# Kernel tuning notes

Hardware: AMD Instinct MI355X
Metric: run time of the kernel (lower is better)

## Reference

```python
import jax, jax.numpy as jnp
import numpy as np

T, B, H = 1024, 128, 256


def setup_inputs() -> dict:
    key = jax.random.key(0)
    k1, k2, k3, k4, k5 = jax.random.split(key, 5)
    ins = jax.random.normal(k1, (T, B, H), dtype=jnp.float32)
    resets = jax.random.randint(k2, (T, B), 0, 2).astype(jnp.bool_)
    # GRUCell params (flax layout): input dense (with bias) and recurrent dense
    # (bias only on the candidate 'hn' branch). Orthogonal-ish init approximated
    # by scaled normal for a pure-jnp reference.
    s = 1.0 / np.sqrt(H)
    Wi = jax.random.normal(k3, (H, 3 * H), dtype=jnp.float32) * s   # -> [ir|iz|in]
    Wh = jax.random.normal(k4, (H, 3 * H), dtype=jnp.float32) * s   # -> [hr|hz|hn]
    bi = jnp.zeros((3 * H,), dtype=jnp.float32)
    bhn = jnp.zeros((H,), dtype=jnp.float32)
    h0 = jnp.zeros((B, H), dtype=jnp.float32)  # initialize_carry -> zeros
    return {"ins": ins, "resets": resets, "h0": h0,
            "Wi": Wi, "Wh": Wh, "bi": bi, "bhn": bhn}


def reference(ins, resets, h0, Wi, Wh, bi, bhn):
    """ScannedRNN: GRU recurrence over time with per-step reset masking.

    ins: [T,B,H], resets: [T,B] bool, h0: [B,H]. Returns (final_carry, ys).
    """
    Hh = h0.shape[-1]

    def step(h, xt):
        x_t, r_t = xt                              # [B,H], [B]
        h = jnp.where(r_t[:, None], 0.0, h)        # reset carry to zeros
        gi = x_t @ Wi + bi                         # [B,3H]
        gh = h @ Wh                                # [B,3H]
        i_r, i_z, i_n = gi[:, :Hh], gi[:, Hh:2 * Hh], gi[:, 2 * Hh:]
        h_r, h_z, h_n = gh[:, :Hh], gh[:, Hh:2 * Hh], gh[:, 2 * Hh:]
        r = jax.nn.sigmoid(i_r + h_r)
        z = jax.nn.sigmoid(i_z + h_z)
        n = jnp.tanh(i_n + r * (h_n + bhn))
        h_new = (1.0 - z) * n + z * h
        return h_new, h_new                        # GRUCell returns (carry, y=carry)

    h_final, ys = jax.lax.scan(step, h0, (ins, resets))
    return h_final, ys
```

## Files before the change

### kernel.cpp

```cpp
#include <hip/hip_runtime.h>


typedef _Float16 half2_t __attribute__((ext_vector_type(2)));
typedef _Float16 half4_t __attribute__((ext_vector_type(4)));
typedef _Float16 half8_t __attribute__((ext_vector_type(8)));
typedef float f32x4 __attribute__((ext_vector_type(4)));

#define T_DIM 1024
#define B_DIM 128
#define H_DIM 256
#define N3 768
#define NSTREAM 4096
#define ROWS 16

__device__ __forceinline__ int perm_n(int cp) {
  int ublk = cp / 48;
  int rem = cp % 48;
  int g = rem >> 4;
  int u4 = rem & 15;
  return g * 256 + ublk * 16 + u4;
}


__global__ void prep_whb(const float* __restrict__ Wh, unsigned* __restrict__ WhB) {
  int i = blockIdx.x * 256 + threadIdx.x;
  int h = 2 * i;
  int idx = h & 7;
  int lane = (h >> 3) & 63;
  int ntk = h >> 9;
  int nt = ntk % 48;
  int kt = ntk / 48;
  int k = kt * 32 + ((lane >> 4) * 8) + idx;
  int n = perm_n(nt * 16 + (lane & 15));
  half2_t p;
  p.x = (_Float16)Wh[(size_t)k * N3 + n];
  p.y = (_Float16)Wh[(size_t)(k + 1) * N3 + n];
  WhB[i] = __builtin_bit_cast(unsigned, p);
}

__global__ void prep_witp(const float* __restrict__ Wi, _Float16* __restrict__ WiTp) {
  int i = blockIdx.x * 256 + threadIdx.x;
  int cp = i >> 8;
  int k = i & 255;
  WiTp[(size_t)cp * 256 + k] = (_Float16)Wi[(size_t)k * N3 + perm_n(cp)];
}

__global__ void prep_bip(const float* __restrict__ bi, float* __restrict__ bip) {
  int i = threadIdx.x;
  bip[i] = bi[perm_n(i)];
}

__global__ void init_h(const float* __restrict__ h0, float* __restrict__ h_state) {
  int i = blockIdx.x * 256 + threadIdx.x;
  h_state[i] = h0[i];
}

__global__ __launch_bounds__(256) void conv_a(
    const float* __restrict__ src, _Float16* __restrict__ dst, int n8) {
  int i = blockIdx.x * 256 + threadIdx.x;
  const int stride = gridDim.x * 256;
  for (; i < n8; i += stride) {
    float4 a = ((const float4*)src)[2 * i];
    float4 b = ((const float4*)src)[2 * i + 1];
    half8_t h;
    h[0] = (_Float16)a.x; h[1] = (_Float16)a.y;
    h[2] = (_Float16)a.z; h[3] = (_Float16)a.w;
    h[4] = (_Float16)b.x; h[5] = (_Float16)b.y;
    h[6] = (_Float16)b.z; h[7] = (_Float16)b.w;
    ((half8_t*)dst)[i] = h;
  }
}


__global__ void seg_transpose(const int* __restrict__ resets, int* __restrict__ resT) {
  int i = blockIdx.x * 256 + threadIdx.x;
  int b = i >> 10;
  int t = i & 1023;
  resT[i] = resets[(size_t)t * B_DIM + b];
}

__global__ __launch_bounds__(256) void seg_extract(
    const int* __restrict__ resT, int t0, int steps,
    unsigned* __restrict__ rowsegs, unsigned* __restrict__ rowcnt,
    unsigned* __restrict__ lhist) {
  const int b = blockIdx.x;
  const int tid = threadIdx.x;
  const int lane = tid & 63;
  const int w = tid >> 6;
  const int per = (steps + 255) >> 8;

  __shared__ unsigned short sstartL[1025];
  __shared__ unsigned lcur[1025];
  __shared__ unsigned wsum[4];

  for (int l = tid; l <= steps; l += 256) lcur[l] = 0;

  const int* rrow = resT + (size_t)b * T_DIM + t0;
  int myfirst = tid * per;
  unsigned cnt = 0;
  for (int i = 0; i < per; ++i) {
    int s = myfirst + i;
    if (s < steps && (s == 0 || rrow[s] != 0)) cnt++;
  }
  unsigned pre = cnt;
#pragma unroll
  for (int off = 1; off < 64; off <<= 1) {
    unsigned v = __shfl_up(pre, off);
    if (lane >= off) pre += v;
  }
  if (lane == 63) wsum[w] = pre;
  __syncthreads();
  unsigned wbase = 0, total = 0;
#pragma unroll
  for (int i = 0; i < 4; ++i) {
    if (i < w) wbase += wsum[i];
    total += wsum[i];
  }
  unsigned r = wbase + pre - cnt;
  for (int i = 0; i < per; ++i) {
    int s = myfirst + i;
    if (s < steps && (s == 0 || rrow[s] != 0)) sstartL[r++] = (unsigned short)s;
  }
  if (tid == 0) { sstartL[total] = (unsigned short)steps; rowcnt[b] = total; }
  __syncthreads();

  const unsigned carry0 = (rrow[0] == 0) ? 1u : 0u;
  for (unsigned rr = tid; rr < total; rr += 256) {
    int st = sstartL[rr];
    int len = (int)sstartL[rr + 1] - st;
    unsigned carry = (st == 0) ? carry0 : 0u;
    unsigned rk = atomicAdd(&lcur[len], 1u);
    rowsegs[(size_t)b * T_DIM + rr] =
        (unsigned)st | ((unsigned)len << 10) | (rk << 21) | (carry << 31);
  }
  __syncthreads();
  for (int l = tid; l <= steps; l += 256) lhist[(size_t)l * 128 + b] = lcur[l];
}

__global__ __launch_bounds__(1024) void seg_prefix2(
    const unsigned* __restrict__ lhist, unsigned* __restrict__ rowoff,
    unsigned* __restrict__ cursors, unsigned* __restrict__ Warr,
    unsigned* __restrict__ nseg, int steps) {
  __shared__ unsigned cs[1024];
  __shared__ unsigned cs2[1024];
  const int tid = threadIdx.x;
  const int len = tid + 1;
  unsigned run = 0;
  if (len <= steps) {
    for (int b = 0; b < 128; ++b) {
      rowoff[(size_t)len * 128 + b] = run;
      run += lhist[(size_t)len * 128 + b];
    }
  }
  unsigned own = run;
  unsigned own2 = run * (unsigned)len;
  cs[tid] = own;
  cs2[tid] = own2;
  for (int off = 1; off < 1024; off <<= 1) {
    __syncthreads();
    unsigned v = (tid + off < 1024) ? cs[tid + off] : 0u;
    unsigned v2 = (tid + off < 1024) ? cs2[tid + off] : 0u;
    __syncthreads();
    cs[tid] += v;
    cs2[tid] += v2;
  }
  cursors[len] = cs[tid] - own;
  Warr[len] = cs2[tid] - own2;
  if (tid == 0) *nseg = cs[0];
}

__global__ void seg_scatter2(
    const unsigned* __restrict__ rowsegs, const unsigned* __restrict__ rowcnt,
    const unsigned* __restrict__ rowoff, const unsigned* __restrict__ cursors,
    unsigned* __restrict__ segs) {
  int i = blockIdx.x * 256 + threadIdx.x;
  int b = i >> 10;
  int rr = i & 1023;
  if ((unsigned)rr >= rowcnt[b]) return;
  unsigned rec = rowsegs[i];
  unsigned st = rec & 0x3FF;
  unsigned len = (rec >> 10) & 0x7FF;
  unsigned rk = (rec >> 21) & 0x3FF;
  unsigned carry = rec >> 31;
  unsigned dst = cursors[len] + rowoff[(size_t)len * 128 + b] + rk;
  segs[dst] = st | (len << 10) | ((unsigned)b << 21) | (carry << 28);
}

__global__ void str_mark(
    const unsigned* __restrict__ segs, const unsigned* __restrict__ nseg_p,
    const unsigned* __restrict__ cursors, const unsigned* __restrict__ Warr,
    unsigned* __restrict__ sstart, unsigned* __restrict__ preexS, int Q) {
  unsigned r = blockIdx.x * 256 + threadIdx.x;
  unsigned n = *nseg_p;
  if (r >= n) return;
  unsigned rec = segs[r];
  unsigned len = (rec >> 10) & 0x7FF;
  unsigned pre = Warr[len] + len * (r - cursors[len]);
  unsigned st = pre / (unsigned)Q;
  unsigned stp;
  if (r == 0) {
    sstart[0] = 0; preexS[0] = 0; stp = 0;
  } else {
    unsigned rec2 = segs[r - 1];
    unsigned len2 = (rec2 >> 10) & 0x7FF;
    unsigned pre2 = Warr[len2] + len2 * (r - 1 - cursors[len2]);
    stp = pre2 / (unsigned)Q;
  }
  for (unsigned s = stp + 1; s <= st; ++s) { sstart[s] = r; preexS[s] = pre; }
}

__global__ __launch_bounds__(256) void gi_gemm(
    const _Float16* __restrict__ A16,
    const _Float16* __restrict__ BT,
    const float* __restrict__ bip,
    _Float16* __restrict__ Cout,
    int M) {
  __shared__ _Float16 Al[128 * 32];
  __shared__ _Float16 Bl[128 * 32];
  const int tid = threadIdx.x;
  const int lane = tid & 63;
  const int w = tid >> 6;
  const int wr = w >> 1, wc = w & 1;
  const int m0 = blockIdx.y * 128;
  const int n0 = blockIdx.x * 128;

  const int srow = lane >> 2;
  const int schunk = lane & 3;

  f32x4 acc[4][4] = {};

  for (int ks = 0; ks < 256; ks += 32) {
#pragma unroll
    for (int rr = 0; rr < 2; ++rr) {
      const int row = w * 32 + rr * 16;
      __builtin_amdgcn_global_load_lds(
          (const __attribute__((address_space(1))) void*)
              ((const char*)A16 + ((size_t)(m0 + row + srow) * 256 + ks) * 2 + schunk * 16),
          (__attribute__((address_space(3))) void*)((char*)Al + row * 64),
          16, 0, 0);
      __builtin_amdgcn_global_load_lds(
          (const __attribute__((address_space(1))) void*)
              ((const char*)BT + ((size_t)(n0 + row + srow) * 256 + ks) * 2 + schunk * 16),
          (__attribute__((address_space(3))) void*)((char*)Bl + row * 64),
          16, 0, 0);
    }
    __syncthreads();

    half8_t af[4], bf[4];
#pragma unroll
    for (int m = 0; m < 4; ++m)
      af[m] = *(const half8_t*)&Al[(size_t)(wr * 64 + m * 16 + (lane & 15)) * 32 + (lane >> 4) * 8];
#pragma unroll
    for (int n = 0; n < 4; ++n)
      bf[n] = *(const half8_t*)&Bl[(size_t)(wc * 64 + n * 16 + (lane & 15)) * 32 + (lane >> 4) * 8];
#pragma unroll
    for (int m = 0; m < 4; ++m)
#pragma unroll
      for (int n = 0; n < 4; ++n)
        acc[m][n] = __builtin_amdgcn_mfma_f32_16x16x32_f16(af[m], bf[n], acc[m][n], 0, 0, 0);
    __syncthreads();
  }

#pragma unroll
  for (int m = 0; m < 4; ++m) {
    int row = m0 + wr * 64 + m * 16 + (lane >> 4) * 4;
#pragma unroll
    for (int n = 0; n < 4; ++n) {
      int col = n0 + wc * 64 + n * 16 + (lane & 15);
      float bv = bip[col];
#pragma unroll
      for (int r2 = 0; r2 < 4; ++r2)
        Cout[(size_t)(row + r2) * N3 + col] = (_Float16)(acc[m][n][r2] + bv);
    }
  }
}

__global__ __launch_bounds__(512)
__attribute__((amdgpu_waves_per_eu(1, 2)))
void scan_stream(
    const _Float16* __restrict__ WhB,
    const _Float16* __restrict__ gi,
    const unsigned* __restrict__ segs,
    const unsigned* __restrict__ sstart,
    const unsigned* __restrict__ preexS,
    const unsigned* __restrict__ nseg_ptr,
    const float* __restrict__ bhn,
    const float* __restrict__ h_in,
    float* __restrict__ h_out,
    float* __restrict__ ys,
    float* __restrict__ hfin,
    float* __restrict__ dump,
    int t0, int steps, int Q) {
  __shared__ _Float16 h_lds[2][ROWS][264];
  __shared__ _Float16 giL[2][ROWS][776];
  __shared__ unsigned rst[ROWS];
  __shared__ unsigned rowrankL[ROWS];
  __shared__ unsigned rowpwL[ROWS];
  __shared__ unsigned wava[8];

  const int tid = threadIdx.x;
  const int lane = tid & 63;
  const int w = tid >> 6;
  const int sbase = blockIdx.x * ROWS;
  const unsigned nseg = *nseg_ptr;
  float* dumpb = dump + (size_t)(blockIdx.x & 63) * 4096;

  if (tid < ROWS) {
    const unsigned st = sbase + tid;
    unsigned r = sstart[st], pw = preexS[st];
    unsigned v = 0u, rk = 0xFFFFFFFFu, rpw0 = 0u;
    if (r < nseg && pw < (st + 1) * (unsigned)Q) {
      unsigned rec = segs[r];
      unsigned len = (rec >> 10) & 0x7FF;
      v = (rec & 0x3FF) | (((rec >> 21) & 0x7F) << 10) | (len << 17) |
          (((rec >> 28) & 1u) << 28);
      rk = r; rpw0 = pw + len;
    }
    rst[tid] = v; rowrankL[tid] = rk; rowpwL[tid] = rpw0;
  }
  if (tid < 8) wava[tid] = 1u;

  half8_t whr[48];
#pragma unroll
  for (int kt = 0; kt < 8; ++kt)
#pragma unroll
    for (int q = 0; q < 6; ++q)
      whr[kt * 6 + q] =
          *(const half8_t*)&WhB[(((size_t)kt * 48 + w * 6 + q) * 64 + lane) * 8];

  __syncthreads();

  unsigned rcur[2], rnxt[2], rrk[2], rpw[2], segnx[2], lim[2];
  unsigned rfr[2];
#pragma unroll
  for (int rr = 0; rr < 2; ++rr) {
    const int row = 2 * w + rr;
    rcur[rr] = rst[row];
    rrk[rr]  = rowrankL[row];
    rpw[rr]  = rowpwL[row];
    lim[rr]  = (unsigned)(sbase + row + 1) * (unsigned)Q;
    unsigned rn2 = rrk[rr] + 1;
    unsigned i2 = (rn2 < nseg) ? rn2 : (nseg - 1);
    segnx[rr] = segs[i2];
  }

#pragma unroll
  for (int rr = 0; rr < 2; ++rr) {
    int row = 2 * w + rr;
    unsigned s = rcur[rr];
    float4 o = make_float4(0.f, 0.f, 0.f, 0.f);
    if (s & (1u << 28))
      o = *(const float4*)&h_in[(size_t)((s >> 10) & 0x7F) * 256 + lane * 4];
    half4_t hv;
    hv.x = (_Float16)o.x; hv.y = (_Float16)o.y;
    hv.z = (_Float16)o.z; hv.w = (_Float16)o.w;
    *(half4_t*)&h_lds[0][row][lane * 4] = hv;
  }

#pragma unroll
  for (int rr = 0; rr < 2; ++rr) {
    const int row = 2 * w + rr;
    const unsigned ss = rcur[rr];
    const int live = (int)((ss >> 17) & 0x7FF);
    const size_t goff = live ? ((size_t)(ss & 0x3FF) * B_DIM + ((ss >> 10) & 0x7F)) * N3 : 0;
    const char* src = (const char*)(gi + goff);
    char* dst = (char*)&giL[0][row][0];
    __builtin_amdgcn_global_load_lds(
        (const __attribute__((address_space(1))) void*)(src + (size_t)lane * 16),
        (__attribute__((address_space(3))) void*)dst, 16, 0, 0);
    __builtin_amdgcn_global_load_lds(
        (const __attribute__((address_space(1))) void*)(src + 1024 + (size_t)lane * 4),
        (__attribute__((address_space(3))) void*)(dst + 1024), 4, 0, 0);
    __builtin_amdgcn_global_load_lds(
        (const __attribute__((address_space(1))) void*)(src + 1280 + (size_t)lane * 4),
        (__attribute__((address_space(3))) void*)(dst + 1280), 4, 0, 0);
  }
#pragma unroll
  for (int rr = 0; rr < 2; ++rr) {
    const int row = 2 * w + rr;
    *(float4*)&dumpb[row * 256 + lane * 4] = make_float4(0.f, 0.f, 0.f, 0.f);
  }

  const int r16 = lane & 15;
  const int q4 = (lane >> 4) * 4;
  const int kq8 = (lane >> 4) * 8;
  const int u0 = w * 32 + r16;
  const float bh0 = bhn[u0];
  const float bh1 = bhn[u0 + 16];

  int cur = 0;
  int hc = 0;
  while (true) {
    asm volatile("s_waitcnt vmcnt(2)" ::: "memory");
    asm volatile("s_waitcnt lgkmcnt(0)" ::: "memory");
    __builtin_amdgcn_s_barrier();
    __builtin_amdgcn_sched_barrier(0);

    unsigned alive = 0;
#pragma unroll
    for (int i = 0; i < 8; ++i) alive += wava[i];
    if (!alive) break;

#pragma unroll
    for (int rr = 0; rr < 2; ++rr) {
      const unsigned cs = rcur[rr];
      const unsigned rem = (cs >> 17) & 0x7FF;
      unsigned nx = 0u;
      rfr[rr] = 0u;
      if (rem > 1) {
        nx = ((cs & 0x3FF) + 1) | (cs & (0x7Fu << 10)) | ((rem - 1) << 17);
      } else if (rem == 1) {
        unsigned rn = rrk[rr] + 1;
        unsigned pw = rpw[rr];
        if (rn < nseg && pw < lim[rr]) {
          unsigned rec = segnx[rr];
          unsigned len = (rec >> 10) & 0x7FF;
          nx = (rec & 0x3FF) | (((rec >> 21) & 0x7F) << 10) | (len << 17) |
               (((rec >> 28) & 1u) << 28);
          rrk[rr] = rn; rpw[rr] = pw + len;
          rfr[rr] = 1u;
          unsigned rn2 = rn + 1;
          unsigned i2 = (rn2 < nseg) ? rn2 : (nseg - 1);
          segnx[rr] = segs[i2];
        }
      }
      rnxt[rr] = nx;
    }

#pragma unroll
    for (int rr = 0; rr < 2; ++rr) {
      const int row = 2 * w + rr;
      const unsigned ss = rnxt[rr];
      const int live = (int)((ss >> 17) & 0x7FF);
      const size_t goff = live ? ((size_t)(ss & 0x3FF) * B_DIM + ((ss >> 10) & 0x7F)) * N3 : 0;
      const char* src = (const char*)(gi + goff);
      char* dst = (char*)&giL[cur ^ 1][row][0];
      __builtin_amdgcn_global_load_lds(
          (const __attribute__((address_space(1))) void*)(src + (size_t)lane * 16),
          (__attribute__((address_space(3))) void*)dst, 16, 0, 0);
      __builtin_amdgcn_global_load_lds(
          (const __attribute__((address_space(1))) void*)(src + 1024 + (size_t)lane * 4),
          (__attribute__((address_space(3))) void*)(dst + 1024), 4, 0, 0);
      __builtin_amdgcn_global_load_lds(
          (const __attribute__((address_space(1))) void*)(src + 1280 + (size_t)lane * 4),
          (__attribute__((address_space(3))) void*)(dst + 1280), 4, 0, 0);
    }

    f32x4 acc[6] = {};
#pragma unroll
    for (int kt = 0; kt < 8; ++kt) {
      half8_t afr = *(const half8_t*)&h_lds[hc][r16][kt * 32 + kq8];
#pragma unroll
      for (int q = 0; q < 6; ++q)
        acc[q] = __builtin_amdgcn_mfma_f32_16x16x32_f16(afr, whr[kt * 6 + q], acc[q], 0, 0, 0);
    }

#pragma unroll
    for (int j = 0; j < 2; ++j) {
      const int u = u0 + j * 16;
      const int cb = w * 96 + j * 48 + r16;
      const float bh = j ? bh1 : bh0;
#pragma unroll
      for (int e = 0; e < 4; ++e) {
        const int row = q4 + e;
        const float gr = (float)giL[cur][row][cb];
        const float gz = (float)giL[cur][row][cb + 16];
        const float gn = (float)giL[cur][row][cb + 32];
        const float sigr = __builtin_amdgcn_rcpf(1.f + __expf(-(gr + acc[3 * j][e])));
        const float sigz = __builtin_amdgcn_rcpf(1.f + __expf(-(gz + acc[3 * j + 1][e])));
        const float narg = fmaf(sigr, acc[3 * j + 2][e] + bh, gn);
        const float eo = __expf(-2.f * narg);
        const float nn = fmaf(2.f, __builtin_amdgcn_rcpf(1.f + eo), -1.f);
        const float hold = (float)h_lds[hc][row][u];
        const float hnew = fmaf(sigz, hold - nn, nn);
        h_lds[hc ^ 1][row][u] = (_Float16)hnew;
      }
    }

    asm volatile("s_waitcnt lgkmcnt(0)" ::: "memory");
    __builtin_amdgcn_s_barrier();
    __builtin_amdgcn_sched_barrier(0);

    unsigned alv = 0;
#pragma unroll
    for (int rr = 0; rr < 2; ++rr) {
      const int row = 2 * w + rr;
      const unsigned sp = rcur[rr];
      const unsigned rem = (sp >> 17) & 0x7FF;
      const int t = sp & 0x3FF;
      const int b = (sp >> 10) & 0x7F;
      half4_t hv = *(const half4_t*)&h_lds[hc ^ 1][row][lane * 4];
      float4 o;
      o.x = (float)hv.x; o.y = (float)hv.y; o.z = (float)hv.z; o.w = (float)hv.w;
      float* ydst = rem
          ? &ys[(((size_t)(t0 + t) * B_DIM + b) * H_DIM) + lane * 4]
          : &dumpb[row * 256 + lane * 4];
      *(float4*)ydst = o;
      if (rem == 1) {
        if (t == steps - 1) *(float4*)&h_out[(size_t)b * 256 + lane * 4] = o;
        if (t0 + t == T_DIM - 1) *(float4*)&hfin[(size_t)b * 256 + lane * 4] = o;
      }
      if ((rnxt[rr] >> 17) & 0x7FF) alv++;
      rcur[rr] = rnxt[rr];
      if (rfr[rr]) {
        unsigned s = rnxt[rr];
        float4 o2 = make_float4(0.f, 0.f, 0.f, 0.f);
        if (s & (1u << 28))
          o2 = *(const float4*)&h_in[(size_t)((s >> 10) & 0x7F) * 256 + lane * 4];
        half4_t hv2;
        hv2.x = (_Float16)o2.x; hv2.y = (_Float16)o2.y;
        hv2.z = (_Float16)o2.z; hv2.w = (_Float16)o2.w;
        *(half4_t*)&h_lds[hc ^ 1][row][lane * 4] = hv2;
      }
    }
    if (lane == 0) wava[w] = alv;

    cur ^= 1;
    hc ^= 1;
  }
}

extern "C" void kernel_launch(void* const* d_in, const int* in_sizes, int n_in,
                              void* d_out, int out_size, void* d_ws, size_t ws_size,
                              hipStream_t stream) {
  const float* ins    = (const float*)d_in[0];
  const int*   resets = (const int*)d_in[1];
  const float* h0     = (const float*)d_in[2];
  const float* Wi     = (const float*)d_in[3];
  const float* Wh     = (const float*)d_in[4];
  const float* bi     = (const float*)d_in[5];
  const float* bhn    = (const float*)d_in[6];
  float* out  = (float*)d_out;
  float* hfin = out;
  float* ys   = out + B_DIM * H_DIM;

  char* ws = (char*)d_ws;
  unsigned*  WhB     = (unsigned*)(ws + 0);
  _Float16*  WiTp    = (_Float16*)(ws + 393216);
  float*     bip     = (float*)(ws + 786432);
  float*     hA      = (float*)(ws + 789504);
  float*     hB      = (float*)(ws + 920576);
  int*       resT    = (int*)(ws + 1051648);
  unsigned*  rowsegs = (unsigned*)(ws + 1575936);
  unsigned*  rowcnt  = (unsigned*)(ws + 2100224);
  unsigned*  lhist   = (unsigned*)(ws + 2100736);
  unsigned*  rowoff  = (unsigned*)(ws + 2625536);
  unsigned*  cursors = (unsigned*)(ws + 3150336);
  unsigned*  Warr    = (unsigned*)(ws + 3154560);
  unsigned*  nseg    = (unsigned*)(ws + 3158784);
  unsigned*  segs    = (unsigned*)(ws + 3158912);
  unsigned*  sstart  = (unsigned*)(ws + 3683200);
  unsigned*  preexS  = (unsigned*)(ws + 3748736);
  float*     dump    = (float*)(ws + 3814400);
  const size_t gi_off = 4862976;

  int CH = T_DIM;
  while (CH > 256) {
    size_t need = gi_off + (size_t)CH * 128 * (N3 + H_DIM) * 2;
    if (need <= ws_size) break;
    CH >>= 1;
  }
  _Float16* gibuf = (_Float16*)(ws + gi_off);
  _Float16* A16   = (_Float16*)(ws + gi_off + (size_t)CH * 128 * N3 * 2);

  prep_whb<<<384, 256, 0, stream>>>(Wh, WhB);
  prep_witp<<<768, 256, 0, stream>>>(Wi, WiTp);
  prep_bip<<<1, 768, 0, stream>>>(bi, bip);
  init_h<<<128, 256, 0, stream>>>(h0, hA);
  seg_transpose<<<512, 256, 0, stream>>>(resets, resT);

  float* hbufs[2] = {hA, hB};
  for (int c = 0, t0 = 0; t0 < T_DIM; ++c, t0 += CH) {
    int steps = (t0 + CH <= T_DIM) ? CH : (T_DIM - t0);
    int M = steps * B_DIM;
    int Q = (M + NSTREAM - 1) / NSTREAM;
    if (Q < 1) Q = 1;

    conv_a<<<2048, 256, 0, stream>>>(ins + (size_t)t0 * B_DIM * H_DIM, A16, M * 32);

    dim3 ggrid(N3 / 128, M / 128);
    gi_gemm<<<ggrid, 256, 0, stream>>>(A16, WiTp, bip, gibuf, M);

    seg_extract<<<128, 256, 0, stream>>>(resT, t0, steps, rowsegs, rowcnt, lhist);
    seg_prefix2<<<1, 1024, 0, stream>>>(lhist, rowoff, cursors, Warr, nseg, steps);
    seg_scatter2<<<512, 256, 0, stream>>>(rowsegs, rowcnt, rowoff, cursors, segs);
    hipMemsetAsync(sstart, 0xFF, 131072, stream);
    str_mark<<<512, 256, 0, stream>>>(segs, nseg, cursors, Warr, sstart, preexS, Q);

    scan_stream<<<NSTREAM / ROWS, 512, 0, stream>>>(
        (const _Float16*)WhB, gibuf, segs, sstart, preexS, nseg, bhn,
        hbufs[c & 1], hbufs[(c + 1) & 1], ys, hfin, dump, t0, steps, Q);
  }
}
```

Baseline: 386.6 us.

## Fuse fp32-to-fp16 input conversion into GEMM and swizzle block order

Drops the separate conv_a kernel that wrote an fp16 copy of the inputs. The GEMM now loads fp32 inputs straight into LDS and converts them to half8 fragments in registers before the MFMA. It also switches to a 1D grid with an XCD-style block swizzle to improve L2 locality. In exchange, LDS traffic for the A tile doubles, and each of the 6 column blocks re-converts the same A rows. The smaller workspace requirement may also let larger time chunks fit.

```diff
diff --git a/kernel.cpp b/kernel.cpp
--- a/kernel.cpp
+++ b/kernel.cpp
@@ -53,22 +53,6 @@
 __global__ void init_h(const float* __restrict__ h0, float* __restrict__ h_state) {
   int i = blockIdx.x * 256 + threadIdx.x;
   h_state[i] = h0[i];
-}
-
-__global__ __launch_bounds__(256) void conv_a(
-    const float* __restrict__ src, _Float16* __restrict__ dst, int n8) {
-  int i = blockIdx.x * 256 + threadIdx.x;
-  const int stride = gridDim.x * 256;
-  for (; i < n8; i += stride) {
-    float4 a = ((const float4*)src)[2 * i];
-    float4 b = ((const float4*)src)[2 * i + 1];
-    half8_t h;
-    h[0] = (_Float16)a.x; h[1] = (_Float16)a.y;
-    h[2] = (_Float16)a.z; h[3] = (_Float16)a.w;
-    h[4] = (_Float16)b.x; h[5] = (_Float16)b.y;
-    h[6] = (_Float16)b.z; h[7] = (_Float16)b.w;
-    ((half8_t*)dst)[i] = h;
-  }
 }
 
 
@@ -210,46 +194,67 @@
 }
 
 __global__ __launch_bounds__(256) void gi_gemm(
-    const _Float16* __restrict__ A16,
+    const float* __restrict__ A,
     const _Float16* __restrict__ BT,
     const float* __restrict__ bip,
     _Float16* __restrict__ Cout,
     int M) {
-  __shared__ _Float16 Al[128 * 32];
+  __shared__ float    Af[128 * 32];
   __shared__ _Float16 Bl[128 * 32];
   const int tid = threadIdx.x;
   const int lane = tid & 63;
   const int w = tid >> 6;
   const int wr = w >> 1, wc = w & 1;
-  const int m0 = blockIdx.y * 128;
-  const int n0 = blockIdx.x * 128;
-
-  const int srow = lane >> 2;
-  const int schunk = lane & 3;
+
+  const int bid = blockIdx.x;
+  const int nwg = gridDim.x;
+  const int swz = (bid & 7) * (nwg >> 3) + (bid >> 3);
+  const int bx = swz % 6;
+  const int by = swz / 6;
+  const int m0 = by * 128;
+  const int n0 = bx * 128;
+
+  const int srowA = lane >> 3;
+  const int schA  = lane & 7;
+  const int srowB = lane >> 2;
+  const int schB  = lane & 3;
 
   f32x4 acc[4][4] = {};
 
   for (int ks = 0; ks < 256; ks += 32) {
 #pragma unroll
-    for (int rr = 0; rr < 2; ++rr) {
-      const int row = w * 32 + rr * 16;
+    for (int g = 0; g < 4; ++g) {
+      const int rowA = w * 32 + g * 8;
       __builtin_amdgcn_global_load_lds(
           (const __attribute__((address_space(1))) void*)
-              ((const char*)A16 + ((size_t)(m0 + row + srow) * 256 + ks) * 2 + schunk * 16),
-          (__attribute__((address_space(3))) void*)((char*)Al + row * 64),
+              ((const char*)A + ((size_t)(m0 + rowA + srowA) * 256 + ks) * 4 + schA * 16),
+          (__attribute__((address_space(3))) void*)((char*)Af + rowA * 128),
           16, 0, 0);
+    }
+#pragma unroll
+    for (int g = 0; g < 2; ++g) {
+      const int rowB = w * 32 + g * 16;
       __builtin_amdgcn_global_load_lds(
           (const __attribute__((address_space(1))) void*)
-              ((const char*)BT + ((size_t)(n0 + row + srow) * 256 + ks) * 2 + schunk * 16),
-          (__attribute__((address_space(3))) void*)((char*)Bl + row * 64),
+              ((const char*)BT + ((size_t)(n0 + rowB + srowB) * 256 + ks) * 2 + schB * 16),
+          (__attribute__((address_space(3))) void*)((char*)Bl + rowB * 64),
           16, 0, 0);
     }
     __syncthreads();
 
     half8_t af[4], bf[4];
 #pragma unroll
-    for (int m = 0; m < 4; ++m)
-      af[m] = *(const half8_t*)&Al[(size_t)(wr * 64 + m * 16 + (lane & 15)) * 32 + (lane >> 4) * 8];
+    for (int m = 0; m < 4; ++m) {
+      const float* ap = &Af[(size_t)(wr * 64 + m * 16 + (lane & 15)) * 32 + (lane >> 4) * 8];
+      float4 a0 = *(const float4*)ap;
+      float4 a1 = *(const float4*)(ap + 4);
+      half8_t h;
+      h[0] = (_Float16)a0.x; h[1] = (_Float16)a0.y;
+      h[2] = (_Float16)a0.z; h[3] = (_Float16)a0.w;
+      h[4] = (_Float16)a1.x; h[5] = (_Float16)a1.y;
+      h[6] = (_Float16)a1.z; h[7] = (_Float16)a1.w;
+      af[m] = h;
+    }
 #pragma unroll
     for (int n = 0; n < 4; ++n)
       bf[n] = *(const half8_t*)&Bl[(size_t)(wc * 64 + n * 16 + (lane & 15)) * 32 + (lane >> 4) * 8];
@@ -556,12 +561,11 @@
 
   int CH = T_DIM;
   while (CH > 256) {
-    size_t need = gi_off + (size_t)CH * 128 * (N3 + H_DIM) * 2;
+    size_t need = gi_off + (size_t)CH * 128 * N3 * 2;
     if (need <= ws_size) break;
     CH >>= 1;
   }
   _Float16* gibuf = (_Float16*)(ws + gi_off);
-  _Float16* A16   = (_Float16*)(ws + gi_off + (size_t)CH * 128 * N3 * 2);
 
   prep_whb<<<384, 256, 0, stream>>>(Wh, WhB);
   prep_witp<<<768, 256, 0, stream>>>(Wi, WiTp);
@@ -576,10 +580,8 @@
     int Q = (M + NSTREAM - 1) / NSTREAM;
     if (Q < 1) Q = 1;
 
-    conv_a<<<2048, 256, 0, stream>>>(ins + (size_t)t0 * B_DIM * H_DIM, A16, M * 32);
-
-    dim3 ggrid(N3 / 128, M / 128);
-    gi_gemm<<<ggrid, 256, 0, stream>>>(A16, WiTp, bip, gibuf, M);
+    gi_gemm<<<6 * (M / 128), 256, 0, stream>>>(
+        ins + (size_t)t0 * B_DIM * H_DIM, WiTp, bip, gibuf, M);
 
     seg_extract<<<128, 256, 0, stream>>>(resT, t0, steps, rowsegs, rowcnt, lhist);
     seg_prefix2<<<1, 1024, 0, stream>>>(lhist, rowoff, cursors, Warr, nseg, steps);
```

New measurement: 528.5 us. 1.37x slower.
